# Kernel optimization log

Hardware: AMD Instinct MI355X
Metric: run time of the kernel (lower is better)

## Reference

```python
import jax, jax.numpy as jnp
import numpy as np
from jax import lax

SHIFT = 32  # shift_range from init
EPS_NORM = 1e-12
EPS_MASK = 1e-6


def _l2_normalize_flat(x):
    # F.normalize(x.reshape(B,-1)): per-sample L2 normalize with eps 1e-12
    B = x.shape[0]
    flat = x.reshape(B, -1)
    n = jnp.linalg.norm(flat, axis=1, keepdims=True)
    return (flat / jnp.maximum(n, EPS_NORM)).reshape(x.shape)


def setup_inputs() -> dict:
    key = jax.random.key(0)
    k1, k2 = jax.random.split(key)
    grd_feature = jax.random.normal(k1, (8, 32, 32, 32), dtype=jnp.float32)
    sat_feature = jax.random.normal(k2, (8, 32, 128, 128), dtype=jnp.float32)
    return {"grd_feature": grd_feature, "sat_feature": sat_feature, "test_method": 1}


def reference(grd_feature, sat_feature, test_method):
    # test_method == 1 path (default); test_method in {0,1} only differ in divisor
    M, C, H_s, W_s = sat_feature.shape
    N, _, H, W = grd_feature.shape
    kH = min(H, H_s - 2 * SHIFT)
    kW = min(W, W_s - 2 * SHIFT)

    # center-crop ground template to (kH, kW) and L2-normalize per sample
    gh0, gw0 = H // 2 - kH // 2, W // 2 - kW // 2
    grd = grd_feature[:, :, gh0:gh0 + 2 * (kH // 2), gw0:gw0 + 2 * (kW // 2)]
    N_, _, H_k, W_k = grd.shape
    grd = _l2_normalize_flat(grd)

    # center-crop satellite to search region and L2-normalize per sample
    sh0 = H_s // 2 - SHIFT - kH // 2
    sw0 = W_s // 2 - SHIFT - kW // 2
    sat = sat_feature[:, :, sh0:sh0 + 2 * (SHIFT + kH // 2), sw0:sw0 + 2 * (SHIFT + kW // 2)]
    _, _, H_i, W_i = sat.shape
    sat = _l2_normalize_flat(sat)

    # all-pairs cross-correlation: corr[m, n, y, x] (torch grouped-conv on repeated sat
    # is equivalent to a plain VALID conv of sat with all N ground filters)
    corr = lax.conv_general_dilated(
        sat, grd, window_strides=(1, 1), padding='VALID',
        dimension_numbers=('NCHW', 'OIHW', 'NCHW'))  # [M, N, Ho, Wo]
    Ho, Wo = corr.shape[2], corr.shape[3]

    # sliding-window sum of |sat|^2 (avg_pool with divisor_override=1, summed over C)
    s2 = jnp.sum(sat * sat, axis=1)  # [M, H_i, W_i]
    partical = lax.reduce_window(s2, jnp.float32(0), lax.add,
                                 (1, H_k, W_k), (1, 1, 1), 'VALID')  # [M, Ho, Wo]
    if test_method == 0:
        denom = jnp.sqrt(partical)
    else:
        denom = partical
    corr = corr / jnp.maximum(denom[:, None], EPS_NORM)

    similarity_matrix = jnp.max(corr, axis=(2, 3))  # [M, N]

    # diagonal pairs (m == n): peak localization
    diag = jnp.diagonal(corr, axis1=0, axis2=1)        # [Ho, Wo, M]
    diag = jnp.transpose(diag, (2, 0, 1)).reshape(M, -1)
    max_index = jnp.argmax(diag, axis=-1)
    pos_h = max_index // Wo
    pos_w = max_index % Wo

    grd_mask = (jnp.abs(jnp.sum(grd, axis=1)) > EPS_MASK).astype(jnp.float32)  # [N, H_k, W_k]

    def place(ph, pw, gm):
        z = jnp.zeros((1, H_i, W_i), dtype=jnp.float32)
        return lax.dynamic_update_slice(z, gm[None], (0, ph, pw))

    mask = jax.vmap(place)(pos_h, pos_w, grd_mask)  # [M, 1, H_i, W_i]
    return similarity_matrix, mask
```

## Files before the change

kernel.cpp:

```cpp
#include <hip/hip_runtime.h>
#include <stdint.h>

typedef unsigned short u16;
typedef unsigned int u32;
typedef unsigned long long u64;
typedef __bf16 bf16x8 __attribute__((ext_vector_type(8)));
typedef float floatx4 __attribute__((ext_vector_type(4)));

#define DEVI static __device__ __forceinline__

DEVI u16 f2bf(float f) {
  uint32_t u = __builtin_bit_cast(uint32_t, f);
  u += 0x7FFFu + ((u >> 16) & 1u);
  return (u16)(u >> 16);
}
DEVI float bf2f(u16 b) { return __builtin_bit_cast(float, (uint32_t)b << 16); }

DEVI u32 encf(float f) {
  u32 u = __builtin_bit_cast(u32, f);
  return (u >> 31) ? ~u : (u | 0x80000000u);
}
DEVI float decf(u32 e) {
  u32 u = (e >> 31) ? (e & 0x7FFFFFFFu) : ~e;
  return __builtin_bit_cast(float, u);
}

DEVI float wred_sum(float v) {
  #pragma unroll
  for (int o = 32; o > 0; o >>= 1) v += __shfl_xor(v, o);
  return v;
}
DEVI float wred_max(float v) {
  #pragma unroll
  for (int o = 32; o > 0; o >>= 1) v = fmaxf(v, __shfl_xor(v, o));
  return v;
}

DEVI void cp16(const u16* g, u16* l) {
#if __has_builtin(__builtin_amdgcn_global_load_lds)
  __builtin_amdgcn_global_load_lds(
      (const __attribute__((address_space(1))) uint32_t*)g,
      (__attribute__((address_space(3))) uint32_t*)l, 16, 0, 0);
#else
  *(uint4*)l = *(const uint4*)g;
#endif
}

static constexpr size_t OFF_CORRP = 0;
static constexpr size_t OFF_SATT  = OFF_CORRP + (size_t)4*270400*4;
static constexpr size_t OFF_GRDP  = OFF_SATT + (size_t)8*4*96*96*8*2;
static constexpr size_t OFF_S2    = OFF_GRDP + (size_t)4*1024*16*8*2;
static constexpr size_t OFF_PART  = OFF_S2   + (size_t)73728*4;
static constexpr size_t OFF_NRMP  = OFF_PART + (size_t)33800*4;
static constexpr size_t OFF_GNRM  = OFF_NRMP + 768*4;
static constexpr size_t OFF_MASK  = OFF_GNRM + 32;
static constexpr size_t OFF_PMAX  = OFF_MASK + (size_t)8192*4;
static constexpr size_t OFF_CNT   = OFF_PMAX + 320*4;
static constexpr size_t OFF_CAND  = OFF_CNT  + 512;

__global__ __launch_bounds__(256) void k_prep(
    const float* __restrict__ grd, const float* __restrict__ sat,
    u16* __restrict__ sTh, u16* __restrict__ gP,
    float* __restrict__ s2, float* __restrict__ nrmp,
    float* __restrict__ gnrm, float* __restrict__ gmask,
    u32* __restrict__ cnts) {
  __shared__ float L[32*100];
  __shared__ float red[4];
  const int t = threadIdx.x;
  if (blockIdx.x < 768) {
    const int m = blockIdx.x / 96, y = blockIdx.x - (blockIdx.x / 96) * 96;
    #pragma unroll
    for (int k = 0; k < 3; ++k) {
      const int idx = k*256 + t;
      const int c = idx / 24, xq = idx - c*24;
      const float4 v = *(const float4*)(sat + (((size_t)m*32 + c)*128 + (16+y))*128 + 16 + xq*4);
      *(float4*)(&L[c*100 + xq*4]) = v;
    }
    __syncthreads();
    float ss = 0.f;
    if (t < 96) {
      #pragma unroll
      for (int c = 0; c < 32; ++c) { const float v = L[c*100 + t]; ss += v*v; }
      s2[(size_t)m*9216 + y*96 + t] = ss;
    }
    const float wsum = wred_sum(ss);
    if ((t & 63) == 0) red[t >> 6] = wsum;
    __syncthreads();
    if (t == 0) nrmp[m*96 + y] = red[0] + red[1] + red[2] + red[3];
    for (int idx = t; idx < 384; idx += 256) {
      const int cb = idx / 96, x = idx - cb*96;
      union { u16 us[8]; uint4 v4; } P;
      #pragma unroll
      for (int e = 0; e < 8; ++e) P.us[e] = f2bf(L[(cb*8+e)*100 + x]);
      *(uint4*)(&sTh[(((size_t)m*4+cb)*9216 + (size_t)y*96 + x)*8]) = P.v4;
    }
  } else if (blockIdx.x == 776) {
    if (t < 72) cnts[t] = 0u;
  } else {
    const int n = blockIdx.x - 768;
    float nn = 0.f, scs[4];
    #pragma unroll
    for (int it = 0; it < 4; ++it) {
      const int pidx = it*256 + t;
      float vals[32]; float sc = 0.f;
      #pragma unroll
      for (int c = 0; c < 32; ++c) {
        const float v = grd[((size_t)n*32 + c)*1024 + pidx];
        vals[c] = v; sc += v; nn += v*v;
      }
      scs[it] = sc;
      #pragma unroll
      for (int cb = 0; cb < 4; ++cb) {
        union { u16 us[8]; uint4 v4; } ph, pl;
        #pragma unroll
        for (int e = 0; e < 8; ++e) {
          const float v = vals[cb*8+e];
          const u16 h = f2bf(v); ph.us[e] = h; pl.us[e] = f2bf(v - bf2f(h));
        }
        const size_t o = ((size_t)cb*1024 + pidx)*128;
        *(uint4*)(&gP[o + (size_t)n*8])     = ph.v4;
        *(uint4*)(&gP[o + (size_t)(n+8)*8]) = pl.v4;
      }
    }
    const float tot = wred_sum(nn);
    if ((t & 63) == 0) red[t >> 6] = tot;
    __syncthreads();
    const float sum = red[0] + red[1] + red[2] + red[3];
    if (t == 0) gnrm[n] = sum;
    const float gn = fmaxf(sqrtf(sum), 1e-12f);
    const float thr = 1e-6f * gn;
    #pragma unroll
    for (int it = 0; it < 4; ++it)
      gmask[n*1024 + it*256 + t] = (fabsf(scs[it]) > thr) ? 1.f : 0.f;
  }
}

__global__ __launch_bounds__(256, 3) void k_conv(
    const u16* __restrict__ satT, const u16* __restrict__ gP,
    const float* __restrict__ s2, float* __restrict__ corr_p,
    float* __restrict__ part)
{
  __shared__ __align__(16) u16 patch[41*48*8];

  const int bi = blockIdx.x;
  const int tid = threadIdx.x;

  if (bi < 72) {
    float* S  = (float*)patch;
    float* HS = S + 40*96;
    const int pm = bi / 9, ysl = (bi - pm*9)*8;
    const int nrows = (65 - ysl) < 8 ? (65 - ysl) : 8;
    const int scnt  = (96 - ysl) < 40 ? (96 - ysl) : 40;
    for (int idx = tid; idx < scnt*96; idx += 256)
      S[idx] = s2[(size_t)pm*9216 + (size_t)ysl*96 + idx];
    __syncthreads();
    const int hrows = nrows + 31;
    for (int idx = tid; idx < hrows*65; idx += 256) {
      const int r = idx / 65, xo = idx - r*65;
      const float* p = &S[r*96 + xo];
      float s = 0.f;
      #pragma unroll
      for (int j = 0; j < 32; ++j) s += p[j];
      HS[idx] = s;
    }
    __syncthreads();
    for (int idx = tid; idx < nrows*65; idx += 256) {
      const int r = idx / 65, xo = idx - r*65;
      float s = 0.f;
      #pragma unroll
      for (int i = 0; i < 32; ++i) s += HS[(r+i)*65 + xo];
      part[(size_t)pm*4225 + (size_t)(ysl+r)*65 + xo] = s;
    }
    return;
  }

  const int wave = tid >> 6, lane = tid & 63;
  const int pr = lane & 15, q = lane >> 4;

  if (bi >= 968) {
    const int e = bi - 968;
    const int cb = e & 3;
    const int yt = (e >> 2) % 5;
    const int m  = e / 20;
    const int ybase = yt * 13;
    const size_t rowbase = ((size_t)(m*4 + cb) * 96 + ybase) * 96;
    for (int k = tid; k < 44*32; k += 256) {
      const int rho = k >> 5, px = k & 31;
      cp16(&satT[(rowbase + (size_t)rho*96 + 64 + px)*8], &patch[(size_t)k*8]);
    }
    asm volatile("s_waitcnt vmcnt(0)" ::: "memory");
    __syncthreads();
    const int prc = pr < 13 ? pr : 12;
    floatx4 acc = (floatx4){0.f, 0.f, 0.f, 0.f};
    #pragma unroll
    for (int jbi = 0; jbi < 2; ++jbi) {
      const int jb = wave*2 + jbi;
      const int px_e = jb*4 + q;
      const u16* bp = gP + ((size_t)cb*1024 + (size_t)(jb*4+q))*128 + (size_t)pr*8;
      uint4 Br[8];
      #pragma unroll
      for (int ii = 0; ii < 8; ++ii) Br[ii] = *(const uint4*)(bp + (size_t)ii*4096);
      uint4 Ah[8];
      #pragma unroll
      for (int s = 0; s < 6; ++s)
        Ah[s] = *(const uint4*)(&patch[((size_t)(prc + s)*32 + px_e)*8]);
      #pragma unroll
      for (int i = 0; i < 32; ++i) {
        if (i < 26)
          Ah[(i+6)&7] = *(const uint4*)(&patch[((size_t)(prc + i + 6)*32 + px_e)*8]);
        const bf16x8 bf = __builtin_bit_cast(bf16x8, Br[i&7]);
        if (i < 24)
          Br[(i+8)&7] = *(const uint4*)(bp + (size_t)(i+8)*4096);
        acc = __builtin_amdgcn_mfma_f32_16x16x32_bf16(
            __builtin_bit_cast(bf16x8, Ah[i&7]), bf, acc, 0, 0, 0);
      }
    }
    float v4[4];
    #pragma unroll
    for (int k = 0; k < 4; ++k) v4[k] = acc[k] + __shfl_xor(acc[k], 8);
    __syncthreads();
    float* red = (float*)patch;
    #pragma unroll
    for (int k = 0; k < 4; ++k) red[((size_t)wave*64 + lane)*5 + k] = v4[k];
    __syncthreads();
    if (wave == 0 && pr < 8) {
      #pragma unroll
      for (int k = 0; k < 4; ++k) {
        const int yoff = q*4 + k;
        if (yoff < 13) {
          float s = 0.f;
          #pragma unroll
          for (int w = 0; w < 4; ++w) s += red[((size_t)w*64 + lane)*5 + k];
          corr_p[(size_t)cb*270400 + ((size_t)(m*8+pr)*65 + (ybase+yoff))*65 + 64] = s;
        }
      }
    }
    return;
  }

  int b = bi - 72;
  const int cb = b & 3; b >>= 2;
  const int xt = b & 3; b >>= 2;
  const int yt = b % 7;
  const int m  = b / 7;
  const int x0 = xt*16;

  if (yt < 6) {
    const int y0 = yt*10;
    const size_t rowbase = ((size_t)(m*4 + cb) * 96 + y0) * 96;
    for (int k = tid; k < 41*48; k += 256) {
      const int rho = k / 48, px = k - (k/48)*48;
      cp16(&satT[(rowbase + (size_t)rho*96 + x0 + px)*8], &patch[(size_t)k*8]);
    }
    asm volatile("s_waitcnt vmcnt(0)" ::: "memory");
    __syncthreads();

    floatx4 acc[10];
    #pragma unroll
    for (int r = 0; r < 10; ++r) acc[r] = (floatx4){0.f, 0.f, 0.f, 0.f};

    #pragma unroll
    for (int jbi = 0; jbi < 2; ++jbi) {
      const int jb = wave*2 + jbi;
      const int apx = pr + jb*4 + q;
      const u16* bp = gP + ((size_t)cb*1024 + (size_t)(jb*4+q))*128 + (size_t)pr*8;

      uint4 Br[8];
      #pragma unroll
      for (int ii = 0; ii < 8; ++ii) Br[ii] = *(const uint4*)(bp + (size_t)ii*4096);
      uint4 Ah[12];
      #pragma unroll
      for (int s = 0; s < 12; ++s) Ah[s] = *(const uint4*)(&patch[((size_t)s*48 + apx)*8]);

      #pragma unroll
      for (int i = 0; i < 32; ++i) {
        const bf16x8 bf = __builtin_bit_cast(bf16x8, Br[i&7]);
        if (i < 24)
          Br[(i+8)&7] = *(const uint4*)(bp + (size_t)(i+8)*4096);
        __builtin_amdgcn_s_setprio(1);
        #pragma unroll
        for (int r = 0; r < 10; ++r)
          acc[r] = __builtin_amdgcn_mfma_f32_16x16x32_bf16(
              __builtin_bit_cast(bf16x8, Ah[(i+r)%12]), bf, acc[r], 0, 0, 0);
        __builtin_amdgcn_s_setprio(0);
        if (i < 29)
          Ah[(i+12)%12] = *(const uint4*)(&patch[((size_t)(i+12)*48 + apx)*8]);
      }
    }

    float* red = (float*)patch;
    #pragma unroll
    for (int half = 0; half < 2; ++half) {
      __syncthreads();
      #pragma unroll
      for (int u = 0; u < 20; ++u)
        red[((size_t)wave*64 + lane)*21 + u] = acc[half*5 + (u>>2)][u&3];
      __syncthreads();
      if (pr < 8) {
        const int fw = wave;
        #pragma unroll
        for (int r = 0; r < 5; ++r) {
          float s = 0.f;
          #pragma unroll
          for (int w = 0; w < 4; ++w)
            s += red[((size_t)w*64 + lane)*21 + r*4 + fw]
               + red[((size_t)w*64 + (lane^8))*21 + r*4 + fw];
          const int x = x0 + q*4 + fw;
          corr_p[(size_t)cb*270400 + ((size_t)(m*8+pr)*65 + (y0 + half*5 + r))*65 + x] = s;
        }
      }
    }
  } else {
    const int y0 = 60;
    const size_t rowbase = ((size_t)(m*4 + cb) * 96 + y0) * 96;
    for (int k = tid; k < 36*48; k += 256) {
      const int rho = k / 48, px = k - (k/48)*48;
      cp16(&satT[(rowbase + (size_t)rho*96 + x0 + px)*8], &patch[(size_t)k*8]);
    }
    asm volatile("s_waitcnt vmcnt(0)" ::: "memory");
    __syncthreads();

    floatx4 acc[5];
    #pragma unroll
    for (int r = 0; r < 5; ++r) acc[r] = (floatx4){0.f, 0.f, 0.f, 0.f};

    #pragma unroll
    for (int jbi = 0; jbi < 2; ++jbi) {
      const int jb = wave*2 + jbi;
      const int apx = pr + jb*4 + q;
      const u16* bp = gP + ((size_t)cb*1024 + (size_t)(jb*4+q))*128 + (size_t)pr*8;

      uint4 Br[8];
      #pragma unroll
      for (int ii = 0; ii < 8; ++ii) Br[ii] = *(const uint4*)(bp + (size_t)ii*4096);
      uint4 Ah[8];
      #pragma unroll
      for (int s = 0; s < 6; ++s) Ah[s] = *(const uint4*)(&patch[((size_t)s*48 + apx)*8]);

      #pragma unroll
      for (int i = 0; i < 32; ++i) {
        if (i < 30)
          Ah[(i+6)&7] = *(const uint4*)(&patch[((size_t)(i+6)*48 + apx)*8]);
        const bf16x8 bf = __builtin_bit_cast(bf16x8, Br[i&7]);
        if (i < 24)
          Br[(i+8)&7] = *(const uint4*)(bp + (size_t)(i+8)*4096);
        __builtin_amdgcn_s_setprio(1);
        #pragma unroll
        for (int r = 0; r < 5; ++r)
          acc[r] = __builtin_amdgcn_mfma_f32_16x16x32_bf16(
              __builtin_bit_cast(bf16x8, Ah[(i+r)&7]), bf, acc[r], 0, 0, 0);
        __builtin_amdgcn_s_setprio(0);
      }
    }

    __syncthreads();
    float* red = (float*)patch;
    #pragma unroll
    for (int u = 0; u < 20; ++u)
      red[((size_t)wave*64 + lane)*21 + u] = acc[u>>2][u&3];
    __syncthreads();
    if (pr < 8) {
      const int fw = wave;
      #pragma unroll
      for (int r = 0; r < 5; ++r) {
        float s = 0.f;
        #pragma unroll
        for (int w = 0; w < 4; ++w)
          s += red[((size_t)w*64 + lane)*21 + r*4 + fw]
             + red[((size_t)w*64 + (lane^8))*21 + r*4 + fw];
        const int x = x0 + q*4 + fw;
        corr_p[(size_t)cb*270400 + ((size_t)(m*8+pr)*65 + (y0+r))*65 + x] = s;
      }
    }
  }
}

__global__ __launch_bounds__(256) void k_post(
    const float* __restrict__ corr_p, const float* __restrict__ part,
    const float* __restrict__ nrmp, const float* __restrict__ gnrm,
    const int* __restrict__ tm, const float* __restrict__ grd,
    const float* __restrict__ sat, const float* __restrict__ gmask,
    u32* __restrict__ pmaxE, u32* __restrict__ grpcnt,
    u32* __restrict__ candcnt, u64* __restrict__ cand,
    float* __restrict__ out)
{
  __shared__ float red[8];
  __shared__ int s_last;
  __shared__ int fidx[128];
  __shared__ u32 fcnt;

  const int bi = blockIdx.x;
  const int m = bi / 40, n = (bi / 5) & 7, yc = bi % 5, g = m*8 + n;
  const int t = threadIdx.x;
  const int wv = t >> 6, ln = t & 63;
  const bool diag = (m == n);

  float v0 = (t < 96) ? nrmp[m*96 + t] : 0.f;
  v0 = wred_sum(v0);
  if (ln == 0) red[wv] = v0;
  __syncthreads();
  const float snrm2 = red[0] + red[1] + red[2] + red[3];
  const float srn = 1.f / fmaxf(sqrtf(snrm2), 1e-12f);
  const float grn = 1.f / fmaxf(sqrtf(gnrm[n]), 1e-12f);
  const float cscale = grn * srn, pscale = srn * srn;
  const int method = tm[0];

  const float* cp = corr_p + (size_t)g*4225;
  const float* pp = part + (size_t)m*4225;
  const int i0 = yc*845, i1 = i0 + 845;
  float vv[4];
  float bestv = -3.4e38f;
  #pragma unroll
  for (int k = 0; k < 4; ++k) {
    const int idx = i0 + k*256 + t;
    float v = -3.4e38f;
    if (idx < i1) {
      const float c = cp[idx] + cp[idx+270400] + cp[idx+540800] + cp[idx+811200];
      const float pt = pp[idx] * pscale;
      float denom = (method == 0) ? sqrtf(pt) : pt;
      denom = fmaxf(denom, 1e-12f);
      v = c * cscale / denom;
    }
    vv[k] = v;
    bestv = fmaxf(bestv, v);
  }
  __syncthreads();
  const float bw = wred_max(bestv);
  if (ln == 0) red[wv] = bw;
  __syncthreads();
  const float bmax = fmaxf(fmaxf(red[0], red[1]), fmaxf(red[2], red[3]));
  if (t == 0) atomicExch(&pmaxE[bi], encf(bmax));
  if (diag) {
    const float lthr = bmax - 3e-3f;
    #pragma unroll
    for (int k = 0; k < 4; ++k) {
      const int idx = i0 + k*256 + t;
      if (idx < i1 && vv[k] >= lthr) {
        const u32 s = atomicAdd(&candcnt[n], 1u);
        if (s < 128)
          atomicExch(&cand[n*128 + s],
                     ((u64)__builtin_bit_cast(u32, vv[k]) << 32) | (u32)idx);
      }
    }
  }
  __syncthreads();
  if (t == 0) s_last = (atomicAdd(&grpcnt[g], 1u) == 4u) ? 1 : 0;
  __syncthreads();
  if (!s_last) return;

  if (t < 5) red[t] = decf(atomicOr(&pmaxE[g*5 + t], 0u));
  __syncthreads();
  const float gmax = fmaxf(fmaxf(fmaxf(red[0], red[1]), fmaxf(red[2], red[3])), red[4]);
  if (t == 0) out[g] = gmax;
  if (!diag) return;

  const float thr = gmax - 3e-3f;
  if (t == 0) fcnt = 0u;
  __syncthreads();
  u32 nc = atomicAdd(&candcnt[n], 0u); if (nc > 128) nc = 128;
  if (t < (int)nc) {
    const u64 pk = atomicAdd(&cand[n*128 + t], 0ULL);
    const float vf = __builtin_bit_cast(float, (u32)(pk >> 32));
    const int idx = (int)(u32)pk;
    if (vf >= thr) { const u32 s = atomicAdd(&fcnt, 1u); fidx[s] = idx; }
  }
  __syncthreads();
  if (t == 0 && fcnt == 0u) { fidx[0] = 0; fcnt = 1u; }
  __syncthreads();
  const int nf = (int)fcnt;

  __shared__ float sbest; __shared__ int sbix;
  if (t == 0) { sbest = -3.4e38f; sbix = 0x7FFFFFFF; }
  __syncthreads();
  const int c = t >> 3, s8 = t & 7;
  for (int ci = 0; ci < nf; ++ci) {
    const int idx = fidx[ci];
    const int y = idx / 65, x = idx - y*65;
    float a = 0.f;
    #pragma unroll
    for (int ii = 0; ii < 4; ++ii) {
      const int i = s8 + ii*8;
      const float* gr = grd + ((size_t)n*32 + c)*1024 + i*32;
      const float* sr = sat + (((size_t)n*32 + c)*128 + (16 + y + i))*128 + (16 + x);
      #pragma unroll
      for (int j = 0; j < 32; ++j) a += gr[j] * sr[j];
    }
    a = wred_sum(a);
    if (ln == 0) red[wv] = a;
    __syncthreads();
    if (t == 0) {
      const float tot = red[0] + red[1] + red[2] + red[3];
      const float pt = part[(size_t)n*4225 + idx] * pscale;
      float denom = (method == 0) ? sqrtf(pt) : pt;
      denom = fmaxf(denom, 1e-12f);
      const float v = tot * cscale / denom;
      if (v > sbest || (v == sbest && idx < sbix)) { sbest = v; sbix = idx; }
    }
    __syncthreads();
  }
  const int bix = sbix;
  const int ph = bix / 65, pw = bix - (bix/65)*65;
  for (int p = t; p < 9216; p += 256) {
    const int yy = p / 96, xx = p - yy*96;
    float val = 0.f;
    if (yy >= ph && yy < ph+32 && xx >= pw && xx < pw+32)
      val = gmask[n*1024 + (yy-ph)*32 + (xx-pw)];
    out[64 + (size_t)n*9216 + p] = val;
  }
}

extern "C" void kernel_launch(void* const* d_in, const int* in_sizes, int n_in,
                              void* d_out, int out_size, void* d_ws, size_t ws_size,
                              hipStream_t stream) {
  const float* grd = (const float*)d_in[0];
  const float* sat = (const float*)d_in[1];
  const int*   tm  = (const int*)d_in[2];
  float* out = (float*)d_out;
  char* ws = (char*)d_ws;

  float* corrp = (float*)(ws + OFF_CORRP);
  u16*   sTh   = (u16*)(ws + OFF_SATT);
  u16*   gP    = (u16*)(ws + OFF_GRDP);
  float* s2    = (float*)(ws + OFF_S2);
  float* part  = (float*)(ws + OFF_PART);
  float* nrmp  = (float*)(ws + OFF_NRMP);
  float* gnrm  = (float*)(ws + OFF_GNRM);
  float* gmask = (float*)(ws + OFF_MASK);
  u32*   pmaxE = (u32*)(ws + OFF_PMAX);
  u32*   cnts  = (u32*)(ws + OFF_CNT);
  u64*   cand  = (u64*)(ws + OFF_CAND);

  k_prep<<<777,  256, 0, stream>>>(grd, sat, sTh, gP, s2, nrmp, gnrm, gmask, cnts);
  k_conv<<<1128, 256, 0, stream>>>(sTh, gP, s2, corrp, part);
  k_post<<<320,  256, 0, stream>>>(corrp, part, nrmp, gnrm, tm, grd, sat, gmask,
                                   pmaxE, cnts, cnts + 64, cand, out);
}
```

Before: 145.6 us.

## Use persistent atomic work queue in conv and distribute diagonal refinement across blocks

The conv kernel now launches 768 persistent blocks that take further tiles from a global atomic ticket counter until all 1128 tiles are done. This is meant to balance uneven tile costs and cut the tail. In the post kernel, each diagonal block now rescores its own local candidates near its block max and publishes the best packed key through a 64-bit atomicMax. Previously the last-arriving block rescored every gathered candidate serially, so this shortens the critical path. In exchange, each tile pays an extra atomic and two barriers, and some candidates are rescored even when they fall below the global threshold.

Result: slower. 154.1 us (+5.8%).

```diff
diff --git a/kernel.cpp b/kernel.cpp
--- a/kernel.cpp
+++ b/kernel.cpp
@@ -56,7 +56,6 @@
 static constexpr size_t OFF_MASK  = OFF_GNRM + 32;
 static constexpr size_t OFF_PMAX  = OFF_MASK + (size_t)8192*4;
 static constexpr size_t OFF_CNT   = OFF_PMAX + 320*4;
-static constexpr size_t OFF_CAND  = OFF_CNT  + 512;
 
 __global__ __launch_bounds__(256) void k_prep(
     const float* __restrict__ grd, const float* __restrict__ sat,
@@ -95,7 +94,7 @@
       *(uint4*)(&sTh[(((size_t)m*4+cb)*9216 + (size_t)y*96 + x)*8]) = P.v4;
     }
   } else if (blockIdx.x == 776) {
-    if (t < 72) cnts[t] = 0u;
+    if (t < 96) cnts[t] = (t == 72) ? 768u : 0u;
   } else {
     const int n = blockIdx.x - 768;
     float nn = 0.f, scs[4];
@@ -138,240 +137,244 @@
 __global__ __launch_bounds__(256, 3) void k_conv(
     const u16* __restrict__ satT, const u16* __restrict__ gP,
     const float* __restrict__ s2, float* __restrict__ corr_p,
-    float* __restrict__ part)
+    float* __restrict__ part, u32* __restrict__ tick)
 {
   __shared__ __align__(16) u16 patch[41*48*8];
-
-  const int bi = blockIdx.x;
+  __shared__ u32 s_bi;
+
   const int tid = threadIdx.x;
-
-  if (bi < 72) {
-    float* S  = (float*)patch;
-    float* HS = S + 40*96;
-    const int pm = bi / 9, ysl = (bi - pm*9)*8;
-    const int nrows = (65 - ysl) < 8 ? (65 - ysl) : 8;
-    const int scnt  = (96 - ysl) < 40 ? (96 - ysl) : 40;
-    for (int idx = tid; idx < scnt*96; idx += 256)
-      S[idx] = s2[(size_t)pm*9216 + (size_t)ysl*96 + idx];
-    __syncthreads();
-    const int hrows = nrows + 31;
-    for (int idx = tid; idx < hrows*65; idx += 256) {
-      const int r = idx / 65, xo = idx - r*65;
-      const float* p = &S[r*96 + xo];
-      float s = 0.f;
-      #pragma unroll
-      for (int j = 0; j < 32; ++j) s += p[j];
-      HS[idx] = s;
-    }
-    __syncthreads();
-    for (int idx = tid; idx < nrows*65; idx += 256) {
-      const int r = idx / 65, xo = idx - r*65;
-      float s = 0.f;
-      #pragma unroll
-      for (int i = 0; i < 32; ++i) s += HS[(r+i)*65 + xo];
-      part[(size_t)pm*4225 + (size_t)(ysl+r)*65 + xo] = s;
-    }
-    return;
-  }
-
   const int wave = tid >> 6, lane = tid & 63;
   const int pr = lane & 15, q = lane >> 4;
 
-  if (bi >= 968) {
-    const int e = bi - 968;
-    const int cb = e & 3;
-    const int yt = (e >> 2) % 5;
-    const int m  = e / 20;
-    const int ybase = yt * 13;
-    const size_t rowbase = ((size_t)(m*4 + cb) * 96 + ybase) * 96;
-    for (int k = tid; k < 44*32; k += 256) {
-      const int rho = k >> 5, px = k & 31;
-      cp16(&satT[(rowbase + (size_t)rho*96 + 64 + px)*8], &patch[(size_t)k*8]);
-    }
-    asm volatile("s_waitcnt vmcnt(0)" ::: "memory");
-    __syncthreads();
-    const int prc = pr < 13 ? pr : 12;
-    floatx4 acc = (floatx4){0.f, 0.f, 0.f, 0.f};
-    #pragma unroll
-    for (int jbi = 0; jbi < 2; ++jbi) {
-      const int jb = wave*2 + jbi;
-      const int px_e = jb*4 + q;
-      const u16* bp = gP + ((size_t)cb*1024 + (size_t)(jb*4+q))*128 + (size_t)pr*8;
-      uint4 Br[8];
-      #pragma unroll
-      for (int ii = 0; ii < 8; ++ii) Br[ii] = *(const uint4*)(bp + (size_t)ii*4096);
-      uint4 Ah[8];
-      #pragma unroll
-      for (int s = 0; s < 6; ++s)
-        Ah[s] = *(const uint4*)(&patch[((size_t)(prc + s)*32 + px_e)*8]);
-      #pragma unroll
-      for (int i = 0; i < 32; ++i) {
-        if (i < 26)
-          Ah[(i+6)&7] = *(const uint4*)(&patch[((size_t)(prc + i + 6)*32 + px_e)*8]);
-        const bf16x8 bf = __builtin_bit_cast(bf16x8, Br[i&7]);
-        if (i < 24)
-          Br[(i+8)&7] = *(const uint4*)(bp + (size_t)(i+8)*4096);
-        acc = __builtin_amdgcn_mfma_f32_16x16x32_bf16(
-            __builtin_bit_cast(bf16x8, Ah[i&7]), bf, acc, 0, 0, 0);
-      }
-    }
-    float v4[4];
-    #pragma unroll
-    for (int k = 0; k < 4; ++k) v4[k] = acc[k] + __shfl_xor(acc[k], 8);
-    __syncthreads();
-    float* red = (float*)patch;
-    #pragma unroll
-    for (int k = 0; k < 4; ++k) red[((size_t)wave*64 + lane)*5 + k] = v4[k];
-    __syncthreads();
-    if (wave == 0 && pr < 8) {
-      #pragma unroll
-      for (int k = 0; k < 4; ++k) {
-        const int yoff = q*4 + k;
-        if (yoff < 13) {
-          float s = 0.f;
-          #pragma unroll
-          for (int w = 0; w < 4; ++w) s += red[((size_t)w*64 + lane)*5 + k];
-          corr_p[(size_t)cb*270400 + ((size_t)(m*8+pr)*65 + (ybase+yoff))*65 + 64] = s;
-        }
-      }
-    }
-    return;
-  }
-
-  int b = bi - 72;
-  const int cb = b & 3; b >>= 2;
-  const int xt = b & 3; b >>= 2;
-  const int yt = b % 7;
-  const int m  = b / 7;
-  const int x0 = xt*16;
-
-  if (yt < 6) {
-    const int y0 = yt*10;
-    const size_t rowbase = ((size_t)(m*4 + cb) * 96 + y0) * 96;
-    for (int k = tid; k < 41*48; k += 256) {
-      const int rho = k / 48, px = k - (k/48)*48;
-      cp16(&satT[(rowbase + (size_t)rho*96 + x0 + px)*8], &patch[(size_t)k*8]);
-    }
-    asm volatile("s_waitcnt vmcnt(0)" ::: "memory");
-    __syncthreads();
-
-    floatx4 acc[10];
-    #pragma unroll
-    for (int r = 0; r < 10; ++r) acc[r] = (floatx4){0.f, 0.f, 0.f, 0.f};
-
-    #pragma unroll
-    for (int jbi = 0; jbi < 2; ++jbi) {
-      const int jb = wave*2 + jbi;
-      const int apx = pr + jb*4 + q;
-      const u16* bp = gP + ((size_t)cb*1024 + (size_t)(jb*4+q))*128 + (size_t)pr*8;
-
-      uint4 Br[8];
-      #pragma unroll
-      for (int ii = 0; ii < 8; ++ii) Br[ii] = *(const uint4*)(bp + (size_t)ii*4096);
-      uint4 Ah[12];
-      #pragma unroll
-      for (int s = 0; s < 12; ++s) Ah[s] = *(const uint4*)(&patch[((size_t)s*48 + apx)*8]);
-
-      #pragma unroll
-      for (int i = 0; i < 32; ++i) {
-        const bf16x8 bf = __builtin_bit_cast(bf16x8, Br[i&7]);
-        if (i < 24)
-          Br[(i+8)&7] = *(const uint4*)(bp + (size_t)(i+8)*4096);
-        __builtin_amdgcn_s_setprio(1);
-        #pragma unroll
-        for (int r = 0; r < 10; ++r)
-          acc[r] = __builtin_amdgcn_mfma_f32_16x16x32_bf16(
-              __builtin_bit_cast(bf16x8, Ah[(i+r)%12]), bf, acc[r], 0, 0, 0);
-        __builtin_amdgcn_s_setprio(0);
-        if (i < 29)
-          Ah[(i+12)%12] = *(const uint4*)(&patch[((size_t)(i+12)*48 + apx)*8]);
-      }
-    }
-
-    float* red = (float*)patch;
-    #pragma unroll
-    for (int half = 0; half < 2; ++half) {
-      __syncthreads();
-      #pragma unroll
-      for (int u = 0; u < 20; ++u)
-        red[((size_t)wave*64 + lane)*21 + u] = acc[half*5 + (u>>2)][u&3];
-      __syncthreads();
-      if (pr < 8) {
-        const int fw = wave;
-        #pragma unroll
-        for (int r = 0; r < 5; ++r) {
-          float s = 0.f;
-          #pragma unroll
-          for (int w = 0; w < 4; ++w)
-            s += red[((size_t)w*64 + lane)*21 + r*4 + fw]
-               + red[((size_t)w*64 + (lane^8))*21 + r*4 + fw];
-          const int x = x0 + q*4 + fw;
-          corr_p[(size_t)cb*270400 + ((size_t)(m*8+pr)*65 + (y0 + half*5 + r))*65 + x] = s;
-        }
-      }
-    }
-  } else {
-    const int y0 = 60;
-    const size_t rowbase = ((size_t)(m*4 + cb) * 96 + y0) * 96;
-    for (int k = tid; k < 36*48; k += 256) {
-      const int rho = k / 48, px = k - (k/48)*48;
-      cp16(&satT[(rowbase + (size_t)rho*96 + x0 + px)*8], &patch[(size_t)k*8]);
-    }
-    asm volatile("s_waitcnt vmcnt(0)" ::: "memory");
-    __syncthreads();
-
-    floatx4 acc[5];
-    #pragma unroll
-    for (int r = 0; r < 5; ++r) acc[r] = (floatx4){0.f, 0.f, 0.f, 0.f};
-
-    #pragma unroll
-    for (int jbi = 0; jbi < 2; ++jbi) {
-      const int jb = wave*2 + jbi;
-      const int apx = pr + jb*4 + q;
-      const u16* bp = gP + ((size_t)cb*1024 + (size_t)(jb*4+q))*128 + (size_t)pr*8;
-
-      uint4 Br[8];
-      #pragma unroll
-      for (int ii = 0; ii < 8; ++ii) Br[ii] = *(const uint4*)(bp + (size_t)ii*4096);
-      uint4 Ah[8];
-      #pragma unroll
-      for (int s = 0; s < 6; ++s) Ah[s] = *(const uint4*)(&patch[((size_t)s*48 + apx)*8]);
-
-      #pragma unroll
-      for (int i = 0; i < 32; ++i) {
-        if (i < 30)
-          Ah[(i+6)&7] = *(const uint4*)(&patch[((size_t)(i+6)*48 + apx)*8]);
-        const bf16x8 bf = __builtin_bit_cast(bf16x8, Br[i&7]);
-        if (i < 24)
-          Br[(i+8)&7] = *(const uint4*)(bp + (size_t)(i+8)*4096);
-        __builtin_amdgcn_s_setprio(1);
-        #pragma unroll
-        for (int r = 0; r < 5; ++r)
-          acc[r] = __builtin_amdgcn_mfma_f32_16x16x32_bf16(
-              __builtin_bit_cast(bf16x8, Ah[(i+r)&7]), bf, acc[r], 0, 0, 0);
-        __builtin_amdgcn_s_setprio(0);
-      }
-    }
-
-    __syncthreads();
-    float* red = (float*)patch;
-    #pragma unroll
-    for (int u = 0; u < 20; ++u)
-      red[((size_t)wave*64 + lane)*21 + u] = acc[u>>2][u&3];
-    __syncthreads();
-    if (pr < 8) {
-      const int fw = wave;
-      #pragma unroll
-      for (int r = 0; r < 5; ++r) {
+  u32 bi = blockIdx.x;
+  for (;;) {
+    if (bi < 72) {
+      float* S  = (float*)patch;
+      float* HS = S + 40*96;
+      const int pm = (int)bi / 9, ysl = ((int)bi - pm*9)*8;
+      const int nrows = (65 - ysl) < 8 ? (65 - ysl) : 8;
+      const int scnt  = (96 - ysl) < 40 ? (96 - ysl) : 40;
+      for (int idx = tid; idx < scnt*96; idx += 256)
+        S[idx] = s2[(size_t)pm*9216 + (size_t)ysl*96 + idx];
+      __syncthreads();
+      const int hrows = nrows + 31;
+      for (int idx = tid; idx < hrows*65; idx += 256) {
+        const int r = idx / 65, xo = idx - r*65;
+        const float* p = &S[r*96 + xo];
         float s = 0.f;
         #pragma unroll
-        for (int w = 0; w < 4; ++w)
-          s += red[((size_t)w*64 + lane)*21 + r*4 + fw]
-             + red[((size_t)w*64 + (lane^8))*21 + r*4 + fw];
-        const int x = x0 + q*4 + fw;
-        corr_p[(size_t)cb*270400 + ((size_t)(m*8+pr)*65 + (y0+r))*65 + x] = s;
-      }
-    }
+        for (int j = 0; j < 32; ++j) s += p[j];
+        HS[idx] = s;
+      }
+      __syncthreads();
+      for (int idx = tid; idx < nrows*65; idx += 256) {
+        const int r = idx / 65, xo = idx - r*65;
+        float s = 0.f;
+        #pragma unroll
+        for (int i = 0; i < 32; ++i) s += HS[(r+i)*65 + xo];
+        part[(size_t)pm*4225 + (size_t)(ysl+r)*65 + xo] = s;
+      }
+    } else if (bi >= 968) {
+      const int e = (int)bi - 968;
+      const int cb = e & 3;
+      const int yt = (e >> 2) % 5;
+      const int m  = e / 20;
+      const int ybase = yt * 13;
+      const size_t rowbase = ((size_t)(m*4 + cb) * 96 + ybase) * 96;
+      for (int k = tid; k < 44*32; k += 256) {
+        const int rho = k >> 5, px = k & 31;
+        cp16(&satT[(rowbase + (size_t)rho*96 + 64 + px)*8], &patch[(size_t)k*8]);
+      }
+      asm volatile("s_waitcnt vmcnt(0)" ::: "memory");
+      __syncthreads();
+      const int prc = pr < 13 ? pr : 12;
+      floatx4 acc = (floatx4){0.f, 0.f, 0.f, 0.f};
+      #pragma unroll
+      for (int jbi = 0; jbi < 2; ++jbi) {
+        const int jb = wave*2 + jbi;
+        const int px_e = jb*4 + q;
+        const u16* bp = gP + ((size_t)cb*1024 + (size_t)(jb*4+q))*128 + (size_t)pr*8;
+        uint4 Br[8];
+        #pragma unroll
+        for (int ii = 0; ii < 8; ++ii) Br[ii] = *(const uint4*)(bp + (size_t)ii*4096);
+        uint4 Ah[8];
+        #pragma unroll
+        for (int s = 0; s < 6; ++s)
+          Ah[s] = *(const uint4*)(&patch[((size_t)(prc + s)*32 + px_e)*8]);
+        #pragma unroll
+        for (int i = 0; i < 32; ++i) {
+          if (i < 26)
+            Ah[(i+6)&7] = *(const uint4*)(&patch[((size_t)(prc + i + 6)*32 + px_e)*8]);
+          const bf16x8 bf = __builtin_bit_cast(bf16x8, Br[i&7]);
+          if (i < 24)
+            Br[(i+8)&7] = *(const uint4*)(bp + (size_t)(i+8)*4096);
+          acc = __builtin_amdgcn_mfma_f32_16x16x32_bf16(
+              __builtin_bit_cast(bf16x8, Ah[i&7]), bf, acc, 0, 0, 0);
+        }
+      }
+      float v4[4];
+      #pragma unroll
+      for (int k = 0; k < 4; ++k) v4[k] = acc[k] + __shfl_xor(acc[k], 8);
+      __syncthreads();
+      float* red = (float*)patch;
+      #pragma unroll
+      for (int k = 0; k < 4; ++k) red[((size_t)wave*64 + lane)*5 + k] = v4[k];
+      __syncthreads();
+      if (wave == 0 && pr < 8) {
+        #pragma unroll
+        for (int k = 0; k < 4; ++k) {
+          const int yoff = q*4 + k;
+          if (yoff < 13) {
+            float s = 0.f;
+            #pragma unroll
+            for (int w = 0; w < 4; ++w) s += red[((size_t)w*64 + lane)*5 + k];
+            corr_p[(size_t)cb*270400 + ((size_t)(m*8+pr)*65 + (ybase+yoff))*65 + 64] = s;
+          }
+        }
+      }
+    } else {
+      int bb = (int)bi - 72;
+      const int cb = bb & 3; bb >>= 2;
+      const int xt = bb & 3; bb >>= 2;
+      const int yt = bb % 7;
+      const int m  = bb / 7;
+      const int x0 = xt*16;
+
+      if (yt < 6) {
+        const int y0 = yt*10;
+        const size_t rowbase = ((size_t)(m*4 + cb) * 96 + y0) * 96;
+        for (int k = tid; k < 41*48; k += 256) {
+          const int rho = k / 48, px = k - (k/48)*48;
+          cp16(&satT[(rowbase + (size_t)rho*96 + x0 + px)*8], &patch[(size_t)k*8]);
+        }
+        asm volatile("s_waitcnt vmcnt(0)" ::: "memory");
+        __syncthreads();
+
+        floatx4 acc[10];
+        #pragma unroll
+        for (int r = 0; r < 10; ++r) acc[r] = (floatx4){0.f, 0.f, 0.f, 0.f};
+
+        #pragma unroll
+        for (int jbi = 0; jbi < 2; ++jbi) {
+          const int jb = wave*2 + jbi;
+          const int apx = pr + jb*4 + q;
+          const u16* bp = gP + ((size_t)cb*1024 + (size_t)(jb*4+q))*128 + (size_t)pr*8;
+
+          uint4 Br[8];
+          #pragma unroll
+          for (int ii = 0; ii < 8; ++ii) Br[ii] = *(const uint4*)(bp + (size_t)ii*4096);
+          uint4 Ah[12];
+          #pragma unroll
+          for (int s = 0; s < 12; ++s) Ah[s] = *(const uint4*)(&patch[((size_t)s*48 + apx)*8]);
+
+          #pragma unroll
+          for (int i = 0; i < 32; ++i) {
+            const bf16x8 bf = __builtin_bit_cast(bf16x8, Br[i&7]);
+            if (i < 24)
+              Br[(i+8)&7] = *(const uint4*)(bp + (size_t)(i+8)*4096);
+            __builtin_amdgcn_s_setprio(1);
+            #pragma unroll
+            for (int r = 0; r < 10; ++r)
+              acc[r] = __builtin_amdgcn_mfma_f32_16x16x32_bf16(
+                  __builtin_bit_cast(bf16x8, Ah[(i+r)%12]), bf, acc[r], 0, 0, 0);
+            __builtin_amdgcn_s_setprio(0);
+            if (i < 29)
+              Ah[(i+12)%12] = *(const uint4*)(&patch[((size_t)(i+12)*48 + apx)*8]);
+          }
+        }
+
+        float* red = (float*)patch;
+        #pragma unroll
+        for (int half = 0; half < 2; ++half) {
+          __syncthreads();
+          #pragma unroll
+          for (int u = 0; u < 20; ++u)
+            red[((size_t)wave*64 + lane)*21 + u] = acc[half*5 + (u>>2)][u&3];
+          __syncthreads();
+          if (pr < 8) {
+            const int fw = wave;
+            #pragma unroll
+            for (int r = 0; r < 5; ++r) {
+              float s = 0.f;
+              #pragma unroll
+              for (int w = 0; w < 4; ++w)
+                s += red[((size_t)w*64 + lane)*21 + r*4 + fw]
+                   + red[((size_t)w*64 + (lane^8))*21 + r*4 + fw];
+              const int x = x0 + q*4 + fw;
+              corr_p[(size_t)cb*270400 + ((size_t)(m*8+pr)*65 + (y0 + half*5 + r))*65 + x] = s;
+            }
+          }
+        }
+      } else {
+        const int y0 = 60;
+        const size_t rowbase = ((size_t)(m*4 + cb) * 96 + y0) * 96;
+        for (int k = tid; k < 36*48; k += 256) {
+          const int rho = k / 48, px = k - (k/48)*48;
+          cp16(&satT[(rowbase + (size_t)rho*96 + x0 + px)*8], &patch[(size_t)k*8]);
+        }
+        asm volatile("s_waitcnt vmcnt(0)" ::: "memory");
+        __syncthreads();
+
+        floatx4 acc[5];
+        #pragma unroll
+        for (int r = 0; r < 5; ++r) acc[r] = (floatx4){0.f, 0.f, 0.f, 0.f};
+
+        #pragma unroll
+        for (int jbi = 0; jbi < 2; ++jbi) {
+          const int jb = wave*2 + jbi;
+          const int apx = pr + jb*4 + q;
+          const u16* bp = gP + ((size_t)cb*1024 + (size_t)(jb*4+q))*128 + (size_t)pr*8;
+
+          uint4 Br[8];
+          #pragma unroll
+          for (int ii = 0; ii < 8; ++ii) Br[ii] = *(const uint4*)(bp + (size_t)ii*4096);
+          uint4 Ah[8];
+          #pragma unroll
+          for (int s = 0; s < 6; ++s) Ah[s] = *(const uint4*)(&patch[((size_t)s*48 + apx)*8]);
+
+          #pragma unroll
+          for (int i = 0; i < 32; ++i) {
+            if (i < 30)
+              Ah[(i+6)&7] = *(const uint4*)(&patch[((size_t)(i+6)*48 + apx)*8]);
+            const bf16x8 bf = __builtin_bit_cast(bf16x8, Br[i&7]);
+            if (i < 24)
+              Br[(i+8)&7] = *(const uint4*)(bp + (size_t)(i+8)*4096);
+            __builtin_amdgcn_s_setprio(1);
+            #pragma unroll
+            for (int r = 0; r < 5; ++r)
+              acc[r] = __builtin_amdgcn_mfma_f32_16x16x32_bf16(
+                  __builtin_bit_cast(bf16x8, Ah[(i+r)&7]), bf, acc[r], 0, 0, 0);
+            __builtin_amdgcn_s_setprio(0);
+          }
+        }
+
+        __syncthreads();
+        float* red = (float*)patch;
+        #pragma unroll
+        for (int u = 0; u < 20; ++u)
+          red[((size_t)wave*64 + lane)*21 + u] = acc[u>>2][u&3];
+        __syncthreads();
+        if (pr < 8) {
+          const int fw = wave;
+          #pragma unroll
+          for (int r = 0; r < 5; ++r) {
+            float s = 0.f;
+            #pragma unroll
+            for (int w = 0; w < 4; ++w)
+              s += red[((size_t)w*64 + lane)*21 + r*4 + fw]
+                 + red[((size_t)w*64 + (lane^8))*21 + r*4 + fw];
+            const int x = x0 + q*4 + fw;
+            corr_p[(size_t)cb*270400 + ((size_t)(m*8+pr)*65 + (y0+r))*65 + x] = s;
+          }
+        }
+      }
+    }
+
+    __syncthreads();
+    if (tid == 0) s_bi = atomicAdd(tick, 1u);
+    __syncthreads();
+    bi = s_bi;
+    if (bi >= 1128) return;
   }
 }
 
@@ -381,13 +384,13 @@
     const int* __restrict__ tm, const float* __restrict__ grd,
     const float* __restrict__ sat, const float* __restrict__ gmask,
     u32* __restrict__ pmaxE, u32* __restrict__ grpcnt,
-    u32* __restrict__ candcnt, u64* __restrict__ cand,
-    float* __restrict__ out)
+    u64* __restrict__ bestu, float* __restrict__ out)
 {
   __shared__ float red[8];
   __shared__ int s_last;
   __shared__ int fidx[128];
   __shared__ u32 fcnt;
+  __shared__ u64 s_bk;
 
   const int bi = blockIdx.x;
   const int m = bi / 40, n = (bi / 5) & 7, yc = bi % 5, g = m*8 + n;
@@ -430,19 +433,53 @@
   __syncthreads();
   const float bmax = fmaxf(fmaxf(red[0], red[1]), fmaxf(red[2], red[3]));
   if (t == 0) atomicExch(&pmaxE[bi], encf(bmax));
+
   if (diag) {
+    if (t == 0) fcnt = 0u;
+    __syncthreads();
     const float lthr = bmax - 3e-3f;
     #pragma unroll
     for (int k = 0; k < 4; ++k) {
       const int idx = i0 + k*256 + t;
       if (idx < i1 && vv[k] >= lthr) {
-        const u32 s = atomicAdd(&candcnt[n], 1u);
-        if (s < 128)
-          atomicExch(&cand[n*128 + s],
-                     ((u64)__builtin_bit_cast(u32, vv[k]) << 32) | (u32)idx);
-      }
-    }
+        const u32 s = atomicAdd(&fcnt, 1u);
+        if (s < 128) fidx[s] = idx;
+      }
+    }
+    __syncthreads();
+    const int nf = (int)(fcnt < 128u ? fcnt : 128u);
+    u64 bestKey = 0ULL;
+    const int c = t >> 3, s8 = t & 7;
+    for (int ci = 0; ci < nf; ++ci) {
+      const int idx = fidx[ci];
+      const int y = idx / 65, x = idx - y*65;
+      float a = 0.f;
+      #pragma unroll
+      for (int ii = 0; ii < 4; ++ii) {
+        const int i = s8 + ii*8;
+        const float* gr = grd + ((size_t)n*32 + c)*1024 + i*32;
+        const float* sr = sat + (((size_t)n*32 + c)*128 + (16 + y + i))*128 + (16 + x);
+        #pragma unroll
+        for (int j = 0; j < 32; ++j) a += gr[j] * sr[j];
+      }
+      a = wred_sum(a);
+      if (ln == 0) red[wv] = a;
+      __syncthreads();
+      if (t == 0) {
+        const float tot = red[0] + red[1] + red[2] + red[3];
+        const float pt = part[(size_t)n*4225 + idx] * pscale;
+        float denom = (method == 0) ? sqrtf(pt) : pt;
+        denom = fmaxf(denom, 1e-12f);
+        const float v = tot * cscale / denom;
+        const u64 key = ((u64)encf(v) << 32) | (u64)(0xFFFFFFFFu - (u32)idx);
+        if (key > bestKey) bestKey = key;
+      }
+      __syncthreads();
+    }
+    if (t == 0 && nf > 0) atomicMax(&bestu[n], bestKey);
+    __threadfence();
   }
+
   __syncthreads();
   if (t == 0) s_last = (atomicAdd(&grpcnt[g], 1u) == 4u) ? 1 : 0;
   __syncthreads();
@@ -454,51 +491,9 @@
   if (t == 0) out[g] = gmax;
   if (!diag) return;
 
-  const float thr = gmax - 3e-3f;
-  if (t == 0) fcnt = 0u;
-  __syncthreads();
-  u32 nc = atomicAdd(&candcnt[n], 0u); if (nc > 128) nc = 128;
-  if (t < (int)nc) {
-    const u64 pk = atomicAdd(&cand[n*128 + t], 0ULL);
-    const float vf = __builtin_bit_cast(float, (u32)(pk >> 32));
-    const int idx = (int)(u32)pk;
-    if (vf >= thr) { const u32 s = atomicAdd(&fcnt, 1u); fidx[s] = idx; }
-  }
-  __syncthreads();
-  if (t == 0 && fcnt == 0u) { fidx[0] = 0; fcnt = 1u; }
-  __syncthreads();
-  const int nf = (int)fcnt;
-
-  __shared__ float sbest; __shared__ int sbix;
-  if (t == 0) { sbest = -3.4e38f; sbix = 0x7FFFFFFF; }
-  __syncthreads();
-  const int c = t >> 3, s8 = t & 7;
-  for (int ci = 0; ci < nf; ++ci) {
-    const int idx = fidx[ci];
-    const int y = idx / 65, x = idx - y*65;
-    float a = 0.f;
-    #pragma unroll
-    for (int ii = 0; ii < 4; ++ii) {
-      const int i = s8 + ii*8;
-      const float* gr = grd + ((size_t)n*32 + c)*1024 + i*32;
-      const float* sr = sat + (((size_t)n*32 + c)*128 + (16 + y + i))*128 + (16 + x);
-      #pragma unroll
-      for (int j = 0; j < 32; ++j) a += gr[j] * sr[j];
-    }
-    a = wred_sum(a);
-    if (ln == 0) red[wv] = a;
-    __syncthreads();
-    if (t == 0) {
-      const float tot = red[0] + red[1] + red[2] + red[3];
-      const float pt = part[(size_t)n*4225 + idx] * pscale;
-      float denom = (method == 0) ? sqrtf(pt) : pt;
-      denom = fmaxf(denom, 1e-12f);
-      const float v = tot * cscale / denom;
-      if (v > sbest || (v == sbest && idx < sbix)) { sbest = v; sbix = idx; }
-    }
-    __syncthreads();
-  }
-  const int bix = sbix;
+  if (t == 0) s_bk = atomicAdd(&bestu[n], 0ULL);
+  __syncthreads();
+  const int bix = (int)(0xFFFFFFFFu - (u32)s_bk);
   const int ph = bix / 65, pw = bix - (bix/65)*65;
   for (int p = t; p < 9216; p += 256) {
     const int yy = p / 96, xx = p - yy*96;
@@ -528,10 +523,11 @@
   float* gmask = (float*)(ws + OFF_MASK);
   u32*   pmaxE = (u32*)(ws + OFF_PMAX);
   u32*   cnts  = (u32*)(ws + OFF_CNT);
-  u64*   cand  = (u64*)(ws + OFF_CAND);
-
-  k_prep<<<777,  256, 0, stream>>>(grd, sat, sTh, gP, s2, nrmp, gnrm, gmask, cnts);
-  k_conv<<<1128, 256, 0, stream>>>(sTh, gP, s2, corrp, part);
-  k_post<<<320,  256, 0, stream>>>(corrp, part, nrmp, gnrm, tm, grd, sat, gmask,
-                                   pmaxE, cnts, cnts + 64, cand, out);
-}
+  u32*   tick  = cnts + 72;
+  u64*   bestu = (u64*)(ws + OFF_CNT + 320);
+
+  k_prep<<<777, 256, 0, stream>>>(grd, sat, sTh, gP, s2, nrmp, gnrm, gmask, cnts);
+  k_conv<<<768, 256, 0, stream>>>(sTh, gP, s2, corrp, part, tick);
+  k_post<<<320, 256, 0, stream>>>(corrp, part, nrmp, gnrm, tm, grd, sat, gmask,
+                                  pmaxE, cnts, bestu, out);
+}
```
